# Kernel tuning notes

Measured on AMD Instinct MI355X. Metric: run time of the kernel, lower is better.

Reference implementation:

```python
import jax, jax.numpy as jnp
import numpy as np
jax.config.update("jax_enable_x64", True)  # original uses float64 internally

B, T, SCALE = 16, 2048, 128


def setup_inputs() -> dict:
    key = jax.random.key(0)
    f0 = jax.random.normal(key, (B, 1, T), dtype=jnp.float32)  # >0 -> voiced
    return {"f0": f0}


def _pchip_upsample(f0, scale):
    Bb, _, Tt = f0.shape
    L = Tt * scale
    up_x = jnp.linspace(0.0, float(Tt - 1), L, dtype=jnp.float64)  # (L,)
    y_full = f0[:, 0, :].astype(jnp.float64)                       # (B,T)
    voiced = y_full > 0.0
    nv = jnp.sum(voiced, axis=1)                                   # (B,) voiced counts

    # --- pack voiced knots to the front (stable argsort: voiced first, in order) ---
    order = jnp.argsort(jnp.logical_not(voiced), axis=1)           # (B,T) int
    x_raw = order.astype(jnp.float64)
    y_raw = jnp.take_along_axis(y_full, order, axis=1)
    pos = jnp.arange(Tt)
    valid = pos[None, :] < nv[:, None]
    last = jnp.maximum(nv - 1, 0)[:, None]
    x_last = jnp.take_along_axis(x_raw, last, axis=1)
    y_last = jnp.take_along_axis(y_raw, last, axis=1)
    # pad x strictly increasing, y constant (=> padded slopes are exactly 0)
    x_p = jnp.where(valid, x_raw, x_last + (pos[None, :] + 1 - nv[:, None]).astype(jnp.float64))
    y_p = jnp.where(valid, y_raw, y_last)

    dx = jnp.diff(x_p, axis=1)                                     # (B,T-1), all > 0
    delta = jnp.diff(y_p, axis=1) / dx

    # --- interior Fritsch-Butland derivatives (weighted harmonic mean) ---
    hk, hkm1 = dx[:, 1:], dx[:, :-1]
    w1 = 2.0 * hk + hkm1
    w2 = hk + 2.0 * hkm1
    dkm1, dk = delta[:, :-1], delta[:, 1:]
    mono = dkm1 * dk > 0.0
    hm = (w1 + w2) / (w1 / jnp.where(mono, dkm1, 1.0) + w2 / jnp.where(mono, dk, 1.0))
    d = jnp.zeros_like(y_p).at[:, 1:-1].set(jnp.where(mono, hm, 0.0))

    # --- endpoint slopes (SciPy one-sided three-point rule + clamps) ---
    h0, h1 = dx[:, 0], dx[:, 1]
    d0 = ((2.0 * h0 + h1) * delta[:, 0] - h0 * delta[:, 1]) / (h0 + h1)
    m0 = d0 * delta[:, 0] <= 0.0
    d0 = jnp.where(m0, 0.0, d0)
    m0b = (delta[:, 0] * delta[:, 1] < 0.0) & ~m0
    d0 = jnp.where(m0b & (jnp.abs(d0) > 3.0 * jnp.abs(delta[:, 0])), 3.0 * delta[:, 0], d0)

    im1 = jnp.clip(nv - 2, 0, Tt - 2)[:, None]
    im2 = jnp.clip(nv - 3, 0, Tt - 2)[:, None]
    hm1 = jnp.take_along_axis(dx, im1, 1)[:, 0]
    hm2 = jnp.take_along_axis(dx, im2, 1)[:, 0]
    dm1 = jnp.take_along_axis(delta, im1, 1)[:, 0]
    dm2 = jnp.take_along_axis(delta, im2, 1)[:, 0]
    dn = ((2.0 * hm1 + hm2) * dm1 - hm1 * dm2) / (hm1 + hm2)
    mn = dn * dm1 <= 0.0
    dn = jnp.where(mn, 0.0, dn)
    mnb = (dm1 * dm2 < 0.0) & ~mn
    dn = jnp.where(mnb & (jnp.abs(dn) > 3.0 * jnp.abs(dm1)), 3.0 * dm1, dn)

    is2 = nv == 2  # exactly two knots -> linear segment
    d0 = jnp.where(is2, delta[:, 0], d0)
    dn = jnp.where(is2, delta[:, 0], dn)
    d = d.at[:, 0].set(d0)
    d = d.at[jnp.arange(Bb), jnp.clip(nv - 1, 0, Tt - 1)].set(dn)

    # --- searchsorted segment lookup + cubic Hermite evaluation ---
    seg = jax.vmap(lambda xv: jnp.searchsorted(xv, up_x, side='right'))(x_p) - 1
    seg = jnp.clip(seg, 0, jnp.maximum(nv - 2, 0)[:, None])        # (B,L)
    x0 = jnp.take_along_axis(x_p, seg, 1)
    x1 = jnp.take_along_axis(x_p, seg + 1, 1)
    y0 = jnp.take_along_axis(y_p, seg, 1)
    y1 = jnp.take_along_axis(y_p, seg + 1, 1)
    g0 = jnp.take_along_axis(d, seg, 1)
    g1 = jnp.take_along_axis(d, seg + 1, 1)
    h = x1 - x0
    t = (up_x[None, :] - x0) / h
    t2 = t * t
    t3 = t2 * t
    up = ((2.0 * t3 - 3.0 * t2 + 1.0) * y0 + (t3 - 2.0 * t2 + t) * h * g0
          + (-2.0 * t3 + 3.0 * t2) * y1 + (t3 - t2) * h * g1)
    up32 = jnp.maximum(up.astype(jnp.float32), 0.0)

    # unvoiced masking via nearest frame index (np round-half-to-even semantics)
    back = jnp.clip(jnp.round(up_x.astype(jnp.float32)).astype(jnp.int32), 0, Tt - 1)
    keep = voiced[:, back] & (nv >= 2)[:, None]
    return jnp.where(keep, up32, 0.0)[:, None, :]


def reference(f0) -> jnp.ndarray:
    return _pchip_upsample(f0, SCALE)
```

## Files before the change

### kernel.cpp

```cpp
#include <hip/hip_runtime.h>


#define TT 2048
#define BB 16
#define LL (TT * 128)
#define CHUNKS 64
#define PTS 4096
#define MAXF 36

typedef float vf4 __attribute__((ext_vector_type(4)));

static constexpr double STEP = 2047.0 / 262143.0;

__global__ __launch_bounds__(256) void pchip_fused(const float* __restrict__ f0,
                                                   float* __restrict__ out) {
    const int b   = blockIdx.x >> 6;
    const int c   = blockIdx.x & 63;
    const int tid = threadIdx.x;
    const int lane = tid & 63;
    const int wv   = tid >> 6;

    __shared__ unsigned short sxs[TT];
    __shared__ float          sys[TT];
    __shared__ unsigned short scnt[TT];
    __shared__ unsigned char  svf[TT];
    __shared__ int            wsum[4];
    __shared__ int            s_nv;
    __shared__ float4         scoef[MAXF];

    const float* y = f0 + b * TT;

    float4 va = reinterpret_cast<const float4*>(y)[tid * 2];
    float4 vb = reinterpret_cast<const float4*>(y)[tid * 2 + 1];
    float vv[8] = {va.x, va.y, va.z, va.w, vb.x, vb.y, vb.z, vb.w};
    const int t8 = tid * 8;
    int cnt = 0;
#pragma unroll
    for (int j = 0; j < 8; ++j) {
        int v = (vv[j] > 0.0f) ? 1 : 0;
        svf[t8 + j] = (unsigned char)v;
        cnt += v;
    }

    int incl = cnt;
#pragma unroll
    for (int off = 1; off < 64; off <<= 1) {
        int n = __shfl_up(incl, off, 64);
        if (lane >= off) incl += n;
    }
    if (lane == 63) wsum[wv] = incl;
    __syncthreads();
    int woff = 0;
    for (int w = 0; w < wv; ++w) woff += wsum[w];
    int run = woff + incl - cnt;

#pragma unroll
    for (int j = 0; j < 8; ++j) {
        if (vv[j] > 0.0f) {
            sxs[run] = (unsigned short)(t8 + j);
            sys[run] = vv[j];
            ++run;
        }
        scnt[t8 + j] = (unsigned short)run;
    }
    if (tid == 255) s_nv = run;
    __syncthreads();

    const int i_base = c * PTS;
    const int tf_lo  = (int)((double)i_base * STEP);
    const int tf_hi  = (int)((double)(i_base + PTS - 1) * STEP);
    const int tlo2   = max(tf_lo - 1, 0);
    const int thi2   = min(tf_hi + 1, TT - 1);
    const int nf     = thi2 - tlo2 + 1;

    const int nv = s_nv;

    if (tid < nf) {
        const int t = tlo2 + tid;
        float4 cf = make_float4(0.f, 0.f, 0.f, 0.f);
        if (nv >= 2) {
            int seg = min(max((int)scnt[t] - 1, 0), nv - 2);

            int p1 = sxs[seg];
            int p2 = sxs[seg + 1];
            float y1v = sys[seg], y2v = sys[seg + 1];
            float h    = (float)(p2 - p1);
            float winv = 1.0f / h;

            float dsg;
            if (nv == 2) {
                dsg = (y2v - y1v) * winv;
            } else if (seg == 0) {
                int p3 = sxs[2];
                float h0 = (float)(p2 - p1), h1 = (float)(p3 - p2);
                float del0 = (y2v - y1v) / h0;
                float del1 = (sys[2] - y2v) / h1;
                float d0 = ((2.0f * h0 + h1) * del0 - h0 * del1) / (h0 + h1);
                if (d0 * del0 <= 0.0f) d0 = 0.0f;
                else if (del0 * del1 < 0.0f && fabsf(d0) > 3.0f * fabsf(del0)) d0 = 3.0f * del0;
                dsg = d0;
            } else {
                int p0 = sxs[seg - 1];
                float hkm1 = (float)(p1 - p0), hk = (float)(p2 - p1);
                float dkm1 = (y1v - sys[seg - 1]) / hkm1;
                float dkk  = (y2v - y1v) / hk;
                if (dkm1 * dkk > 0.0f) {
                    float w1 = 2.0f * hk + hkm1, w2 = hk + 2.0f * hkm1;
                    dsg = (w1 + w2) / (w1 / dkm1 + w2 / dkk);
                } else dsg = 0.0f;
            }

            float dsg1;
            if (nv == 2) {
                dsg1 = (y2v - y1v) * winv;
            } else if (seg + 1 == nv - 1) {
                int p0 = sxs[seg - 1];
                float hm1 = (float)(p2 - p1), hm2 = (float)(p1 - p0);
                float dm1 = (y2v - y1v) / hm1;
                float dm2 = (y1v - sys[seg - 1]) / hm2;
                float dn = ((2.0f * hm1 + hm2) * dm1 - hm1 * dm2) / (hm1 + hm2);
                if (dn * dm1 <= 0.0f) dn = 0.0f;
                else if (dm1 * dm2 < 0.0f && fabsf(dn) > 3.0f * fabsf(dm1)) dn = 3.0f * dm1;
                dsg1 = dn;
            } else {
                int p3 = sxs[seg + 2];
                float hkm1 = (float)(p2 - p1), hk = (float)(p3 - p2);
                float dkm1 = (y2v - y1v) / hkm1;
                float dkk  = (sys[seg + 2] - y2v) / hk;
                if (dkm1 * dkk > 0.0f) {
                    float w1 = 2.0f * hk + hkm1, w2 = hk + 2.0f * hkm1;
                    dsg1 = (w1 + w2) / (w1 / dkm1 + w2 / dkk);
                } else dsg1 = 0.0f;
            }

            float hg0 = h * dsg, hg1 = h * dsg1;
            float D  = y2v - y1v;
            float b1 = hg0;
            float b2 = 3.0f * D - 2.0f * hg0 - hg1;
            float b3 = hg0 + hg1 - 2.0f * D;
            float t0 = ((float)t - (float)p1) * winv;
            float a0 = ((b3 * t0 + b2) * t0 + b1) * t0 + y1v;
            float a1 = winv * ((3.0f * b3 * t0 + 2.0f * b2) * t0 + b1);
            float a2 = winv * winv * (b2 + 3.0f * b3 * t0);
            float a3 = winv * winv * winv * b3;

            unsigned k0 = svf[t];
            unsigned k1 = svf[min(t + 1, TT - 1)];
            unsigned ua3 = (__float_as_uint(a3) & ~3u) | k0 | (k1 << 1);
            cf = make_float4(a0, a1, a2, __uint_as_float(ua3));
        }
        scoef[tid] = cf;
    }
    __syncthreads();

    vf4* og = reinterpret_cast<vf4*>(out + (size_t)b * LL + i_base);
#pragma unroll
    for (int g = 0; g < 4; ++g) {
        const int ii = g * 1024 + tid * 4;
        const int ib = i_base + ii;
        float r[4];
        float4 a = make_float4(0.f, 0.f, 0.f, 0.f);
        int tf_cur = -1;
#pragma unroll
        for (int j = 0; j < 4; ++j) {
            double ux = (double)(ib + j) * STEP;
            float uxf = (float)ux;
            int tf = (int)uxf;
            if (tf != tf_cur) {
                a = scoef[tf - tlo2];
                tf_cur = tf;
            }
            float u = uxf - (float)tf;
            unsigned kc = __float_as_uint(a.w) & 3u;
            float up = fmaf(u, fmaf(u, fmaf(u, a.w, a.z), a.y), a.x);
            up = fmaxf(up, 0.0f);
            int back = (int)rintf(uxf);
            unsigned kb = (kc >> (back - tf)) & 1u;
            r[j] = kb ? up : 0.0f;
        }
        vf4 rv = {r[0], r[1], r[2], r[3]};
        __builtin_nontemporal_store(rv, &og[ii >> 2]);
    }
}

extern "C" void kernel_launch(void* const* d_in, const int* in_sizes, int n_in,
                              void* d_out, int out_size, void* d_ws, size_t ws_size,
                              hipStream_t stream) {
    const float* f0 = (const float*)d_in[0];
    float* out = (float*)d_out;
    pchip_fused<<<BB * CHUNKS, 256, 0, stream>>>(f0, out);
}
```

Measured before the change: 11.60 us.

## Precompute sample positions before scan to overlap with load latency; vectorize scnt writes

Moves the per-output fp64 position computation (fractional offset, frame index, rounding code) ahead of the voiced-count scan so it can overlap with the global load latency and the barriers. The results are packed into registers for the final evaluation loop. The scnt writes become a single 16-byte shared store. The nontemporal output store is replaced by a regular float4 store. In exchange it holds more live registers (16 floats plus 4 packed words) across the barriers and changes the store cache policy.

```diff
diff --git a/kernel.cpp b/kernel.cpp
--- a/kernel.cpp
+++ b/kernel.cpp
@@ -32,39 +32,6 @@
 
     float4 va = reinterpret_cast<const float4*>(y)[tid * 2];
     float4 vb = reinterpret_cast<const float4*>(y)[tid * 2 + 1];
-    float vv[8] = {va.x, va.y, va.z, va.w, vb.x, vb.y, vb.z, vb.w};
-    const int t8 = tid * 8;
-    int cnt = 0;
-#pragma unroll
-    for (int j = 0; j < 8; ++j) {
-        int v = (vv[j] > 0.0f) ? 1 : 0;
-        svf[t8 + j] = (unsigned char)v;
-        cnt += v;
-    }
-
-    int incl = cnt;
-#pragma unroll
-    for (int off = 1; off < 64; off <<= 1) {
-        int n = __shfl_up(incl, off, 64);
-        if (lane >= off) incl += n;
-    }
-    if (lane == 63) wsum[wv] = incl;
-    __syncthreads();
-    int woff = 0;
-    for (int w = 0; w < wv; ++w) woff += wsum[w];
-    int run = woff + incl - cnt;
-
-#pragma unroll
-    for (int j = 0; j < 8; ++j) {
-        if (vv[j] > 0.0f) {
-            sxs[run] = (unsigned short)(t8 + j);
-            sys[run] = vv[j];
-            ++run;
-        }
-        scnt[t8 + j] = (unsigned short)run;
-    }
-    if (tid == 255) s_nv = run;
-    __syncthreads();
 
     const int i_base = c * PTS;
     const int tf_lo  = (int)((double)i_base * STEP);
@@ -72,6 +39,64 @@
     const int tlo2   = max(tf_lo - 1, 0);
     const int thi2   = min(tf_hi + 1, TT - 1);
     const int nf     = thi2 - tlo2 + 1;
+
+    float    pu[16];
+    unsigned pk[4] = {0u, 0u, 0u, 0u};
+#pragma unroll
+    for (int g = 0; g < 4; ++g) {
+#pragma unroll
+        for (int j = 0; j < 4; ++j) {
+            const int idx = g * 4 + j;
+            const int il  = g * 1024 + tid * 4 + j;
+            double ux = (double)(i_base + il) * STEP;
+            float uxf = (float)ux;
+            int tf = (int)uxf;
+            pu[idx] = uxf - (float)tf;
+            int back = (int)rintf(uxf);
+            unsigned code = (unsigned)((tf - tlo2) << 1) | (unsigned)(back - tf);
+            pk[idx >> 2] |= code << (8 * (idx & 3));
+        }
+    }
+
+    float vv[8] = {va.x, va.y, va.z, va.w, vb.x, vb.y, vb.z, vb.w};
+    const int t8 = tid * 8;
+    int cnt = 0;
+#pragma unroll
+    for (int j = 0; j < 8; ++j) {
+        int v = (vv[j] > 0.0f) ? 1 : 0;
+        svf[t8 + j] = (unsigned char)v;
+        cnt += v;
+    }
+
+    int incl = cnt;
+#pragma unroll
+    for (int off = 1; off < 64; off <<= 1) {
+        int n = __shfl_up(incl, off, 64);
+        if (lane >= off) incl += n;
+    }
+    if (lane == 63) wsum[wv] = incl;
+    __syncthreads();
+    int woff = 0;
+    for (int w = 0; w < wv; ++w) woff += wsum[w];
+    int run = woff + incl - cnt;
+
+    unsigned scp[4];
+#pragma unroll
+    for (int m = 0; m < 4; ++m) {
+        unsigned lo, hi;
+        {
+            int j = 2 * m;
+            if (vv[j] > 0.0f) { sxs[run] = (unsigned short)(t8 + j); sys[run] = vv[j]; ++run; }
+            lo = (unsigned)run;
+            ++j;
+            if (vv[j] > 0.0f) { sxs[run] = (unsigned short)(t8 + j); sys[run] = vv[j]; ++run; }
+            hi = (unsigned)run;
+        }
+        scp[m] = lo | (hi << 16);
+    }
+    *reinterpret_cast<uint4*>(&scnt[t8]) = make_uint4(scp[0], scp[1], scp[2], scp[3]);
+    if (tid == 255) s_nv = run;
+    __syncthreads();
 
     const int nv = s_nv;
 
@@ -153,33 +178,30 @@
     }
     __syncthreads();
 
-    vf4* og = reinterpret_cast<vf4*>(out + (size_t)b * LL + i_base);
+    float4* og = reinterpret_cast<float4*>(out + (size_t)b * LL + i_base);
 #pragma unroll
     for (int g = 0; g < 4; ++g) {
         const int ii = g * 1024 + tid * 4;
-        const int ib = i_base + ii;
         float r[4];
         float4 a = make_float4(0.f, 0.f, 0.f, 0.f);
-        int tf_cur = -1;
+        int tfr_cur = -1;
 #pragma unroll
         for (int j = 0; j < 4; ++j) {
-            double ux = (double)(ib + j) * STEP;
-            float uxf = (float)ux;
-            int tf = (int)uxf;
-            if (tf != tf_cur) {
-                a = scoef[tf - tlo2];
-                tf_cur = tf;
+            const int idx = g * 4 + j;
+            unsigned code = (pk[idx >> 2] >> (8 * (idx & 3))) & 0xffu;
+            int tfr = (int)(code >> 1);
+            if (tfr != tfr_cur) {
+                a = scoef[tfr];
+                tfr_cur = tfr;
             }
-            float u = uxf - (float)tf;
+            float u = pu[idx];
             unsigned kc = __float_as_uint(a.w) & 3u;
             float up = fmaf(u, fmaf(u, fmaf(u, a.w, a.z), a.y), a.x);
             up = fmaxf(up, 0.0f);
-            int back = (int)rintf(uxf);
-            unsigned kb = (kc >> (back - tf)) & 1u;
+            unsigned kb = (kc >> (code & 1u)) & 1u;
             r[j] = kb ? up : 0.0f;
         }
-        vf4 rv = {r[0], r[1], r[2], r[3]};
-        __builtin_nontemporal_store(rv, &og[ii >> 2]);
+        og[ii >> 2] = make_float4(r[0], r[1], r[2], r[3]);
     }
 }
 
```

Result: slower. 13.22 us (+13.9%).
